# Kernel tuning notes

Measured on AMD Instinct MI355X. Metric: run time of the kernel, lower is better.

## Reference

```python
import jax, jax.numpy as jnp
import numpy as np

B, H, W, C = 64, 56, 56, 128
HEADS, WS, SHIFT = 4, 7, 3
HID = 4 * C
EPS = 1e-5
WS2 = WS * WS
DH = C // HEADS
# padding per torch code: [P_l, P_r, P_t, P_b] = [ws-shift, shift, ws-shift, shift]
P_L, P_R, P_T, P_B = WS - SHIFT, SHIFT, WS - SHIFT, SHIFT
_H, _W = H + P_T + P_B, W + P_L + P_R  # 63, 63


def layer_norm(x, g, b):
    mu = jnp.mean(x, axis=-1, keepdims=True)
    xc = x - mu
    var = jnp.mean(xc * xc, axis=-1, keepdims=True)
    return xc * jax.lax.rsqrt(var + EPS) * g + b


def setup_inputs() -> dict:
    key = jax.random.key(0)
    ks = jax.random.split(key, 12)
    s = 0.02
    return {
        "x": jax.random.normal(ks[0], (B, H * W, C), jnp.float32),
        "g1": jnp.ones((C,), jnp.float32),
        "b1": jnp.zeros((C,), jnp.float32),
        "spatial_w": jax.random.normal(ks[1], (HEADS, WS2, WS2), jnp.float32) * s,
        "spatial_b": jnp.zeros((HEADS, WS2), jnp.float32),
        "g2": jnp.ones((C,), jnp.float32),
        "b2": jnp.zeros((C,), jnp.float32),
        "fc1_w": jax.random.normal(ks[2], (C, HID), jnp.float32) * s,
        "fc1_b": jnp.zeros((HID,), jnp.float32),
        "fc2_w": jax.random.normal(ks[3], (HID, C), jnp.float32) * s,
        "fc2_b": jnp.zeros((C,), jnp.float32),
    }


def reference(x, g1, b1, spatial_w, spatial_b, g2, b2, fc1_w, fc1_b, fc2_w, fc2_b):
    shortcut = x
    xn = layer_norm(x, g1, b1).reshape(B, H, W, C)
    # shifted padding (shift_size > 0 branch)
    xp = jnp.pad(xn, ((0, 0), (P_T, P_B), (P_L, P_R), (0, 0)))  # (B,_H,_W,C)
    nh, nw = _H // WS, _W // WS
    # window_partition -> (B*nh*nw, WS*WS, C)
    xw = xp.reshape(B, nh, WS, nw, WS, C).transpose(0, 1, 3, 2, 4, 5).reshape(-1, WS2, C)
    # split heads: (nWB, HEADS, WS2, DH)
    xh = xw.reshape(-1, WS2, HEADS, DH).transpose(0, 2, 1, 3)
    # grouped 1x1 Conv1d == per-head token-mixing matmul over the WS2 axis
    yh = jnp.einsum("bhjd,hij->bhid", xh, spatial_w) + spatial_b[None, :, :, None]
    yw = yh.transpose(0, 2, 1, 3).reshape(-1, WS2, C)
    # window_reverse -> (B,_H,_W,C), then crop the shift padding
    y = yw.reshape(B, nh, nw, WS, WS, C).transpose(0, 1, 3, 2, 4, 5).reshape(B, _H, _W, C)
    y = y[:, P_T:_H - P_B, P_L:_W - P_R, :].reshape(B, H * W, C)
    x = shortcut + y
    # channel MLP with exact (erf) GELU as in F.gelu
    h = layer_norm(x, g2, b2)
    h = jax.nn.gelu(h @ fc1_w + fc1_b, approximate=False)
    x = x + (h @ fc2_w + fc2_b)
    return x
```

## Files before the change

### kernel.cpp

```cpp
#include <hip/hip_runtime.h>

typedef unsigned short u16;
typedef __attribute__((ext_vector_type(8))) short short8;
typedef __attribute__((ext_vector_type(4))) float floatx4;

#define NB 64
#define HH 56
#define WW_ 56
#define CC 128
#define NHEADS 4
#define WS2 49
#define PAD 4
#define HID 512

__device__ __forceinline__ float bf2f(u16 u){ return __uint_as_float(((unsigned)u)<<16); }
__device__ __forceinline__ u16 f2bf(float f){
  unsigned u = __float_as_uint(f);
  return (u16)((u + 0x7FFFu + ((u>>16)&1u)) >> 16);
}
__device__ __forceinline__ unsigned pk2(float a, float b){
  return ((unsigned)f2bf(b) << 16) | (unsigned)f2bf(a);
}
__device__ __forceinline__ float gelu_f(float x){
  float u2 = x*(1.5957691216f + 0.0713548162f*x*x);
  return x / (1.f + __expf(-u2));
}
__device__ __forceinline__ short8 ld_frag(const u16* p){
  short8 v;
  #pragma unroll
  for (int e = 0; e < 8; e++) v[e] = (short)p[e];
  return v;
}

__global__ __launch_bounds__(256) void prep_k(
    const float* __restrict__ fc1_w, const float* __restrict__ fc2_w,
    const float* __restrict__ sw,
    u16* __restrict__ fc1_wT, u16* __restrict__ fc2_wT, u16* __restrict__ swT)
{
  int tid = blockIdx.x*256 + threadIdx.x;
  int nth = gridDim.x * 256;
  for (int idx = tid; idx < HID*CC; idx += nth) {
    int n = idx >> 7, k = idx & 127;
    fc1_wT[idx] = f2bf(fc1_w[k*HID + n]);
  }
  for (int idx = tid; idx < CC*HID; idx += nth) {
    int c = idx >> 9, h = idx & 511;
    fc2_wT[idx] = f2bf(fc2_w[h*CC + c]);
  }
  for (int idx = tid; idx < NHEADS*64*72; idx += nth) {
    int hd = idx / (64*72); int rem = idx - hd*64*72;
    int i = rem / 72, j = rem - i*72;
    swT[idx] = (i < WS2 && j < WS2) ? f2bf(sw[(hd*WS2 + i)*WS2 + j]) : (u16)0;
  }
}

__global__ __launch_bounds__(256, 3) void winmix_k(
    const float* __restrict__ x, const float* __restrict__ g1, const float* __restrict__ b1,
    const u16* __restrict__ swT, const float* __restrict__ sb,
    float* __restrict__ x2)
{
  __shared__ __align__(16) char uw[NHEADS*64*72*2];
  __shared__ float sbl[NHEADS*WS2];
  u16* wl  = (u16*)uw;
  u16* xnt = (u16*)uw;
  int tid = threadIdx.x;
  int wvid = tid >> 6, lane = tid & 63;
  int ln = lane & 15, qd = lane >> 4;
  int b = blockIdx.x / 81; int wi = blockIdx.x - b*81;
  int wh = wi / 9, wwn = wi - wh*9;

  {
    const uint2* ws = (const uint2*)swT;
    uint2* wd = (uint2*)wl;
    #pragma unroll
    for (int r = 0; r < 18; r++) wd[tid + r*256] = ws[tid + r*256];
    if (tid < NHEADS*WS2) sbl[tid] = sb[tid];
  }
  __syncthreads();

  int hd = wvid;
  const u16* wbase = wl + hd*64*72;
  short8 af[4][2];
  #pragma unroll
  for (int mt = 0; mt < 4; mt++)
    #pragma unroll
    for (int ks = 0; ks < 2; ks++)
      af[mt][ks] = ld_frag(&wbase[(mt*16 + ln)*72 + ks*32 + qd*8]);
  __syncthreads();

  float gl0 = g1[lane], gl1 = g1[lane+64];
  float bl0 = b1[lane], bl1 = b1[lane+64];
  for (int jj = wvid; jj < 64; jj += 4) {
    u16 o0 = 0, o1 = 0;
    if (jj < WS2) {
      int jr = jj / 7, jc = jj - jr*7;
      int pr = wh*7 + jr - PAD, pc = wwn*7 + jc - PAD;
      bool valid = (pr>=0) & (pr<HH) & (pc>=0) & (pc<WW_);
      float v0 = 0.f, v1 = 0.f;
      const float* px = x + ((size_t)((b*HH + pr)*WW_ + pc))*CC;
      if (valid) { v0 = px[lane]; v1 = px[lane+64]; }
      float s = v0 + v1, ss = v0*v0 + v1*v1;
      #pragma unroll
      for (int o = 32; o > 0; o >>= 1) { s += __shfl_xor(s, o); ss += __shfl_xor(ss, o); }
      float mu = s * (1.f/128.f);
      float var = ss * (1.f/128.f) - mu*mu;
      float rs = rsqrtf(var + 1e-5f);
      if (valid) {
        o0 = f2bf((v0 - mu)*rs*gl0 + bl0);
        o1 = f2bf((v1 - mu)*rs*gl1 + bl1);
      }
    }
    xnt[lane*66 + jj]      = o0;
    xnt[(lane+64)*66 + jj] = o1;
  }
  __syncthreads();

  short8 bf_[2][2];
  #pragma unroll
  for (int nt = 0; nt < 2; nt++)
    #pragma unroll
    for (int ks = 0; ks < 2; ks++)
      bf_[nt][ks] = ld_frag(&xnt[(hd*32 + nt*16 + ln)*66 + ks*32 + qd*8]);
  floatx4 acc[4][2];
  #pragma unroll
  for (int mt = 0; mt < 4; mt++)
    #pragma unroll
    for (int nt = 0; nt < 2; nt++)
      acc[mt][nt] = (floatx4){0.f,0.f,0.f,0.f};
  #pragma unroll
  for (int ks = 0; ks < 2; ks++)
    #pragma unroll
    for (int mt = 0; mt < 4; mt++)
      #pragma unroll
      for (int nt = 0; nt < 2; nt++)
        acc[mt][nt] = __builtin_amdgcn_mfma_f32_16x16x32_bf16(af[mt][ks], bf_[nt][ks], acc[mt][nt], 0, 0, 0);

  #pragma unroll
  for (int mt = 0; mt < 4; mt++) {
    #pragma unroll
    for (int r = 0; r < 4; r++) {
      int i = mt*16 + qd*4 + r;
      if (i < WS2) {
        int ir = i / 7, ic = i - ir*7;
        int orow = wh*7 + ir - PAD, ocol = wwn*7 + ic - PAD;
        if (orow>=0 && orow<HH && ocol>=0 && ocol<WW_) {
          float sbv = sbl[hd*WS2 + i];
          size_t base = ((size_t)((b*HH + orow)*WW_ + ocol))*CC + hd*32;
          #pragma unroll
          for (int nt = 0; nt < 2; nt++) {
            int c = nt*16 + ln;
            x2[base + c] = x[base + c] + acc[mt][nt][r] + sbv;
          }
        }
      }
    }
  }
}

__global__ __launch_bounds__(256, 3) void mlp_k(
    float* __restrict__ xio,
    const float* __restrict__ g2, const float* __restrict__ b2,
    const u16* __restrict__ fc1_wT, const float* __restrict__ fc1_b,
    const u16* __restrict__ fc2_wT, const float* __restrict__ fc2_b)
{
  __shared__ __align__(16) char um[53248];
  u16* ALn = (u16*)um;
  u16* B1p = (u16*)um;
  u16* B2p = (u16*)(um + 17408);
  int tid = threadIdx.x;
  int wvid = tid >> 6, lane = tid & 63;
  int ln = lane & 15, qd = lane >> 4;
  int m0 = wvid*32;
  size_t tokbase = (size_t)blockIdx.x * 128;
  u16* Htp = (u16*)(um + 35840) + wvid*(32*68);

  const uint4* src1 = (const uint4*)fc1_wT;
  const uint4* src2 = (const uint4*)fc2_wT;
  uint4 p1[4], p2[4];
  int n1[4], q1[4], n2[4], q2[4];
  #pragma unroll
  for (int r = 0; r < 4; r++) {
    int idx = tid + r*256;
    n1[r] = idx >> 4; q1[r] = idx & 15;
    n2[r] = idx >> 3; q2[r] = idx & 7;
  }
  auto load_ch = [&](int cc){
    #pragma unroll
    for (int r = 0; r < 4; r++) {
      p1[r] = src1[(cc*64 + n1[r])*16 + q1[r]];
      p2[r] = src2[n2[r]*64 + cc*8 + q2[r]];
    }
  };
  auto store_ch = [&](){
    uint4* d1 = (uint4*)B1p; uint4* d2 = (uint4*)B2p;
    #pragma unroll
    for (int r = 0; r < 4; r++) {
      d1[n1[r]*17 + q1[r]] = p1[r];
      d2[n2[r]*9  + q2[r]] = p2[r];
    }
  };
  load_ch(0);

  float2 gl = *(const float2*)&g2[2*lane];
  float2 bl = *(const float2*)&b2[2*lane];
  for (int t = wvid; t < 128; t += 4) {
    float2 v = *(const float2*)(xio + (tokbase + t)*CC + 2*lane);
    float s = v.x + v.y, ss = v.x*v.x + v.y*v.y;
    #pragma unroll
    for (int o = 32; o > 0; o >>= 1) { s += __shfl_xor(s,o); ss += __shfl_xor(ss,o); }
    float mu = s*(1.f/128.f), var = ss*(1.f/128.f) - mu*mu;
    float rs = rsqrtf(var + 1e-5f);
    *(unsigned*)&ALn[t*136 + 2*lane] =
        pk2((v.x-mu)*rs*gl.x + bl.x, (v.y-mu)*rs*gl.y + bl.y);
  }
  __syncthreads();

  short8 bv[2][4];
  #pragma unroll
  for (int n = 0; n < 2; n++)
    #pragma unroll
    for (int ks = 0; ks < 4; ks++)
      bv[n][ks] = ld_frag(&ALn[(m0 + n*16 + ln)*136 + ks*32 + qd*8]);
  __syncthreads();

  store_ch();
  __syncthreads();

  floatx4 oacc[2][8];
  #pragma unroll
  for (int mt = 0; mt < 2; mt++)
    #pragma unroll
    for (int nt = 0; nt < 8; nt++) oacc[mt][nt] = (floatx4){0.f,0.f,0.f,0.f};

  for (int ch = 0; ch < 8; ch++) {
    if (ch < 7) load_ch(ch+1);

    #pragma unroll
    for (int kt = 0; kt < 4; ++kt) {
      short8 aw[4];
      #pragma unroll
      for (int ks = 0; ks < 4; ks++)
        aw[ks] = ld_frag(&B1p[(kt*16 + ln)*136 + ks*32 + qd*8]);
      floatx4 h0 = (floatx4){0.f,0.f,0.f,0.f};
      floatx4 h1 = (floatx4){0.f,0.f,0.f,0.f};
      #pragma unroll
      for (int ks = 0; ks < 4; ks++) {
        h0 = __builtin_amdgcn_mfma_f32_16x16x32_bf16(aw[ks], bv[0][ks], h0, 0, 0, 0);
        h1 = __builtin_amdgcn_mfma_f32_16x16x32_bf16(aw[ks], bv[1][ks], h1, 0, 0, 0);
      }
      floatx4 bias = *(const floatx4*)&fc1_b[ch*64 + kt*16 + qd*4];
      uint2 u0, u1;
      u0.x = pk2(gelu_f(h0[0]+bias[0]), gelu_f(h0[1]+bias[1]));
      u0.y = pk2(gelu_f(h0[2]+bias[2]), gelu_f(h0[3]+bias[3]));
      u1.x = pk2(gelu_f(h1[0]+bias[0]), gelu_f(h1[1]+bias[1]));
      u1.y = pk2(gelu_f(h1[2]+bias[2]), gelu_f(h1[3]+bias[3]));
      *(uint2*)&Htp[(     ln)*68 + kt*16 + qd*4] = u0;
      *(uint2*)&Htp[(16 + ln)*68 + kt*16 + qd*4] = u1;
    }

    short8 av2[2][2];
    #pragma unroll
    for (int mt = 0; mt < 2; mt++)
      #pragma unroll
      for (int ks = 0; ks < 2; ks++)
        av2[mt][ks] = ld_frag(&Htp[(mt*16 + ln)*68 + ks*32 + qd*8]);
    #pragma unroll
    for (int nt = 0; nt < 8; nt++) {
      short8 bv2[2];
      #pragma unroll
      for (int ks = 0; ks < 2; ks++)
        bv2[ks] = ld_frag(&B2p[(nt*16 + ln)*72 + ks*32 + qd*8]);
      #pragma unroll
      for (int mt = 0; mt < 2; mt++)
        #pragma unroll
        for (int ks = 0; ks < 2; ks++)
          oacc[mt][nt] = __builtin_amdgcn_mfma_f32_16x16x32_bf16(av2[mt][ks], bv2[ks], oacc[mt][nt], 0, 0, 0);
    }
    __syncthreads();
    if (ch < 7) { store_ch(); __syncthreads(); }
  }

  float bias2[8];
  #pragma unroll
  for (int nt = 0; nt < 8; nt++) bias2[nt] = fc2_b[nt*16 + ln];
  #pragma unroll
  for (int mt = 0; mt < 2; mt++)
    #pragma unroll
    for (int r = 0; r < 4; r++) {
      size_t tok = tokbase + m0 + mt*16 + qd*4 + r;
      float* rowp = xio + tok*CC;
      #pragma unroll
      for (int nt = 0; nt < 8; nt++) {
        int n = nt*16 + ln;
        rowp[n] = rowp[n] + oacc[mt][nt][r] + bias2[nt];
      }
    }
}

extern "C" void kernel_launch(void* const* d_in, const int* in_sizes, int n_in,
                              void* d_out, int out_size, void* d_ws, size_t ws_size,
                              hipStream_t stream) {
  const float* x     = (const float*)d_in[0];
  const float* g1    = (const float*)d_in[1];
  const float* b1    = (const float*)d_in[2];
  const float* sw    = (const float*)d_in[3];
  const float* sb    = (const float*)d_in[4];
  const float* g2    = (const float*)d_in[5];
  const float* b2    = (const float*)d_in[6];
  const float* fc1_w = (const float*)d_in[7];
  const float* fc1_b = (const float*)d_in[8];
  const float* fc2_w = (const float*)d_in[9];
  const float* fc2_b = (const float*)d_in[10];
  float* out = (float*)d_out;

  u16* fc1_wT = (u16*)d_ws;
  u16* fc2_wT = fc1_wT + HID*CC;
  u16* swT    = fc2_wT + CC*HID;

  prep_k<<<64, 256, 0, stream>>>(fc1_w, fc2_w, sw, fc1_wT, fc2_wT, swT);
  winmix_k<<<NB*81, 256, 0, stream>>>(x, g1, b1, swT, sb, out);
  mlp_k<<<(NB*HH*WW_)/128, 256, 0, stream>>>(out, g2, b2, fc1_wT, fc1_b, fc2_wT, fc2_b);
}
```

Baseline: 500.6 us.

## Keep GELU output in registers for fc2 MFMA and drop LDS staging

The MLP kernel now packs the GELU results into bf16 MFMA B-operands directly in registers, using the hardware pack-convert instruction. This removes the per-wave LDS hidden-tile write and read-back, and the fc2 accumulator is transposed so the output can be written with vector floatx4 stores. The winmix kernel loads its mixing weights straight from global memory instead of staging them in LDS and reads the bias from global, with the weight padding changed to 80. LDS is smaller, but occupancy hints shift (mlp 3 to 2, winmix 3 to 4), and the GELU division becomes a reciprocal multiply with slightly different rounding.

Result: slower. 531.7 us (+6.2%).

```diff
diff --git a/kernel.cpp b/kernel.cpp
--- a/kernel.cpp
+++ b/kernel.cpp
@@ -2,6 +2,8 @@
 
 typedef unsigned short u16;
 typedef __attribute__((ext_vector_type(8))) short short8;
+typedef __attribute__((ext_vector_type(4))) short short4v;
+typedef __attribute__((ext_vector_type(2))) unsigned uint2v;
 typedef __attribute__((ext_vector_type(4))) float floatx4;
 
 #define NB 64
@@ -21,14 +23,36 @@
 __device__ __forceinline__ unsigned pk2(float a, float b){
   return ((unsigned)f2bf(b) << 16) | (unsigned)f2bf(a);
 }
+__device__ __forceinline__ short4v pk4(float a, float b, float c, float d){
+  unsigned w0, w1;
+  asm("v_cvt_pk_bf16_f32 %0, %1, %2" : "=v"(w0) : "v"(a), "v"(b));
+  asm("v_cvt_pk_bf16_f32 %0, %1, %2" : "=v"(w1) : "v"(c), "v"(d));
+  uint2v u; u[0] = w0; u[1] = w1;
+  return __builtin_bit_cast(short4v, u);
+}
 __device__ __forceinline__ float gelu_f(float x){
   float u2 = x*(1.5957691216f + 0.0713548162f*x*x);
-  return x / (1.f + __expf(-u2));
+  return x * __builtin_amdgcn_rcpf(1.f + __expf(-u2));
 }
 __device__ __forceinline__ short8 ld_frag(const u16* p){
   short8 v;
   #pragma unroll
   for (int e = 0; e < 8; e++) v[e] = (short)p[e];
+  return v;
+}
+__device__ __forceinline__ short4v ld_frag4(const u16* p){
+  short4v v;
+  #pragma unroll
+  for (int e = 0; e < 4; e++) v[e] = (short)p[e];
+  return v;
+}
+__device__ __forceinline__ short8 ld_frag_g(const u16* p){
+  return *(const short8*)p;
+}
+__device__ __forceinline__ short8 cat8(short4v lo, short4v hi){
+  short8 v;
+  #pragma unroll
+  for (int e = 0; e < 4; e++) { v[e] = lo[e]; v[e+4] = hi[e]; }
   return v;
 }
 
@@ -47,71 +71,57 @@
     int c = idx >> 9, h = idx & 511;
     fc2_wT[idx] = f2bf(fc2_w[h*CC + c]);
   }
-  for (int idx = tid; idx < NHEADS*64*72; idx += nth) {
-    int hd = idx / (64*72); int rem = idx - hd*64*72;
-    int i = rem / 72, j = rem - i*72;
+  for (int idx = tid; idx < NHEADS*64*80; idx += nth) {
+    int hd = idx / (64*80); int rem = idx - hd*64*80;
+    int i = rem / 80, j = rem - i*80;
     swT[idx] = (i < WS2 && j < WS2) ? f2bf(sw[(hd*WS2 + i)*WS2 + j]) : (u16)0;
   }
 }
 
-__global__ __launch_bounds__(256, 3) void winmix_k(
+__global__ __launch_bounds__(256, 4) void winmix_k(
     const float* __restrict__ x, const float* __restrict__ g1, const float* __restrict__ b1,
     const u16* __restrict__ swT, const float* __restrict__ sb,
     float* __restrict__ x2)
 {
-  __shared__ __align__(16) char uw[NHEADS*64*72*2];
-  __shared__ float sbl[NHEADS*WS2];
-  u16* wl  = (u16*)uw;
-  u16* xnt = (u16*)uw;
+  __shared__ u16 xnt[CC*66];
   int tid = threadIdx.x;
   int wvid = tid >> 6, lane = tid & 63;
   int ln = lane & 15, qd = lane >> 4;
   int b = blockIdx.x / 81; int wi = blockIdx.x - b*81;
   int wh = wi / 9, wwn = wi - wh*9;
-
-  {
-    const uint2* ws = (const uint2*)swT;
-    uint2* wd = (uint2*)wl;
-    #pragma unroll
-    for (int r = 0; r < 18; r++) wd[tid + r*256] = ws[tid + r*256];
-    if (tid < NHEADS*WS2) sbl[tid] = sb[tid];
-  }
-  __syncthreads();
-
   int hd = wvid;
-  const u16* wbase = wl + hd*64*72;
+
   short8 af[4][2];
   #pragma unroll
   for (int mt = 0; mt < 4; mt++)
     #pragma unroll
     for (int ks = 0; ks < 2; ks++)
-      af[mt][ks] = ld_frag(&wbase[(mt*16 + ln)*72 + ks*32 + qd*8]);
-  __syncthreads();
-
-  float gl0 = g1[lane], gl1 = g1[lane+64];
-  float bl0 = b1[lane], bl1 = b1[lane+64];
+      af[mt][ks] = ld_frag_g(&swT[(size_t)(hd*64 + mt*16 + ln)*80 + ks*32 + qd*8]);
+
+  float2 gl = *(const float2*)&g1[2*lane];
+  float2 bl = *(const float2*)&b1[2*lane];
   for (int jj = wvid; jj < 64; jj += 4) {
     u16 o0 = 0, o1 = 0;
     if (jj < WS2) {
       int jr = jj / 7, jc = jj - jr*7;
       int pr = wh*7 + jr - PAD, pc = wwn*7 + jc - PAD;
       bool valid = (pr>=0) & (pr<HH) & (pc>=0) & (pc<WW_);
-      float v0 = 0.f, v1 = 0.f;
+      float2 v = {0.f, 0.f};
       const float* px = x + ((size_t)((b*HH + pr)*WW_ + pc))*CC;
-      if (valid) { v0 = px[lane]; v1 = px[lane+64]; }
-      float s = v0 + v1, ss = v0*v0 + v1*v1;
+      if (valid) v = *(const float2*)(px + 2*lane);
+      float s = v.x + v.y, ss = v.x*v.x + v.y*v.y;
       #pragma unroll
       for (int o = 32; o > 0; o >>= 1) { s += __shfl_xor(s, o); ss += __shfl_xor(ss, o); }
       float mu = s * (1.f/128.f);
       float var = ss * (1.f/128.f) - mu*mu;
       float rs = rsqrtf(var + 1e-5f);
       if (valid) {
-        o0 = f2bf((v0 - mu)*rs*gl0 + bl0);
-        o1 = f2bf((v1 - mu)*rs*gl1 + bl1);
+        o0 = f2bf((v.x - mu)*rs*gl.x + bl.x);
+        o1 = f2bf((v.y - mu)*rs*gl.y + bl.y);
       }
     }
-    xnt[lane*66 + jj]      = o0;
-    xnt[(lane+64)*66 + jj] = o1;
+    xnt[(2*lane  )*66 + jj] = o0;
+    xnt[(2*lane+1)*66 + jj] = o1;
   }
   __syncthreads();
 
@@ -144,7 +154,7 @@
         int ir = i / 7, ic = i - ir*7;
         int orow = wh*7 + ir - PAD, ocol = wwn*7 + ic - PAD;
         if (orow>=0 && orow<HH && ocol>=0 && ocol<WW_) {
-          float sbv = sbl[hd*WS2 + i];
+          float sbv = sb[hd*WS2 + i];
           size_t base = ((size_t)((b*HH + orow)*WW_ + ocol))*CC + hd*32;
           #pragma unroll
           for (int nt = 0; nt < 2; nt++) {
@@ -157,13 +167,13 @@
   }
 }
 
-__global__ __launch_bounds__(256, 3) void mlp_k(
+__global__ __launch_bounds__(256, 2) void mlp_k(
     float* __restrict__ xio,
     const float* __restrict__ g2, const float* __restrict__ b2,
     const u16* __restrict__ fc1_wT, const float* __restrict__ fc1_b,
     const u16* __restrict__ fc2_wT, const float* __restrict__ fc2_b)
 {
-  __shared__ __align__(16) char um[53248];
+  __shared__ __align__(16) char um[35840];
   u16* ALn = (u16*)um;
   u16* B1p = (u16*)um;
   u16* B2p = (u16*)(um + 17408);
@@ -172,7 +182,6 @@
   int ln = lane & 15, qd = lane >> 4;
   int m0 = wvid*32;
   size_t tokbase = (size_t)blockIdx.x * 128;
-  u16* Htp = (u16*)(um + 35840) + wvid*(32*68);
 
   const uint4* src1 = (const uint4*)fc1_wT;
   const uint4* src2 = (const uint4*)fc2_wT;
@@ -226,75 +235,64 @@
   store_ch();
   __syncthreads();
 
-  floatx4 oacc[2][8];
-  #pragma unroll
-  for (int mt = 0; mt < 2; mt++)
-    #pragma unroll
-    for (int nt = 0; nt < 8; nt++) oacc[mt][nt] = (floatx4){0.f,0.f,0.f,0.f};
+  floatx4 oacc[8][2];
+  #pragma unroll
+  for (int nt = 0; nt < 8; nt++)
+    #pragma unroll
+    for (int th = 0; th < 2; th++) oacc[nt][th] = (floatx4){0.f,0.f,0.f,0.f};
 
   for (int ch = 0; ch < 8; ch++) {
     if (ch < 7) load_ch(ch+1);
 
     #pragma unroll
-    for (int kt = 0; kt < 4; ++kt) {
-      short8 aw[4];
+    for (int kb = 0; kb < 2; ++kb) {
+      short4v pkv[2][2];
       #pragma unroll
-      for (int ks = 0; ks < 4; ks++)
-        aw[ks] = ld_frag(&B1p[(kt*16 + ln)*136 + ks*32 + qd*8]);
-      floatx4 h0 = (floatx4){0.f,0.f,0.f,0.f};
-      floatx4 h1 = (floatx4){0.f,0.f,0.f,0.f};
+      for (int kp = 0; kp < 2; ++kp) {
+        int kt = kb*2 + kp;
+        short8 aw[4];
+        #pragma unroll
+        for (int ks = 0; ks < 4; ks++)
+          aw[ks] = ld_frag(&B1p[(kt*16 + ln)*136 + ks*32 + qd*8]);
+        floatx4 h0 = (floatx4){0.f,0.f,0.f,0.f};
+        floatx4 h1 = (floatx4){0.f,0.f,0.f,0.f};
+        #pragma unroll
+        for (int ks = 0; ks < 4; ks++) {
+          h0 = __builtin_amdgcn_mfma_f32_16x16x32_bf16(aw[ks], bv[0][ks], h0, 0, 0, 0);
+          h1 = __builtin_amdgcn_mfma_f32_16x16x32_bf16(aw[ks], bv[1][ks], h1, 0, 0, 0);
+        }
+        floatx4 bias = *(const floatx4*)&fc1_b[ch*64 + kt*16 + qd*4];
+        pkv[kp][0] = pk4(gelu_f(h0[0]+bias[0]), gelu_f(h0[1]+bias[1]),
+                         gelu_f(h0[2]+bias[2]), gelu_f(h0[3]+bias[3]));
+        pkv[kp][1] = pk4(gelu_f(h1[0]+bias[0]), gelu_f(h1[1]+bias[1]),
+                         gelu_f(h1[2]+bias[2]), gelu_f(h1[3]+bias[3]));
+      }
+      short8 g0 = cat8(pkv[0][0], pkv[1][0]);
+      short8 g1 = cat8(pkv[0][1], pkv[1][1]);
       #pragma unroll
-      for (int ks = 0; ks < 4; ks++) {
-        h0 = __builtin_amdgcn_mfma_f32_16x16x32_bf16(aw[ks], bv[0][ks], h0, 0, 0, 0);
-        h1 = __builtin_amdgcn_mfma_f32_16x16x32_bf16(aw[ks], bv[1][ks], h1, 0, 0, 0);
+      for (int nt = 0; nt < 8; nt++) {
+        const u16* wrow = &B2p[(nt*16 + ln)*72 + kb*32 + qd*4];
+        short8 aw2 = cat8(ld_frag4(wrow), ld_frag4(wrow + 16));
+        oacc[nt][0] = __builtin_amdgcn_mfma_f32_16x16x32_bf16(aw2, g0, oacc[nt][0], 0, 0, 0);
+        oacc[nt][1] = __builtin_amdgcn_mfma_f32_16x16x32_bf16(aw2, g1, oacc[nt][1], 0, 0, 0);
       }
-      floatx4 bias = *(const floatx4*)&fc1_b[ch*64 + kt*16 + qd*4];
-      uint2 u0, u1;
-      u0.x = pk2(gelu_f(h0[0]+bias[0]), gelu_f(h0[1]+bias[1]));
-      u0.y = pk2(gelu_f(h0[2]+bias[2]), gelu_f(h0[3]+bias[3]));
-      u1.x = pk2(gelu_f(h1[0]+bias[0]), gelu_f(h1[1]+bias[1]));
-      u1.y = pk2(gelu_f(h1[2]+bias[2]), gelu_f(h1[3]+bias[3]));
-      *(uint2*)&Htp[(     ln)*68 + kt*16 + qd*4] = u0;
-      *(uint2*)&Htp[(16 + ln)*68 + kt*16 + qd*4] = u1;
-    }
-
-    short8 av2[2][2];
-    #pragma unroll
-    for (int mt = 0; mt < 2; mt++)
-      #pragma unroll
-      for (int ks = 0; ks < 2; ks++)
-        av2[mt][ks] = ld_frag(&Htp[(mt*16 + ln)*68 + ks*32 + qd*8]);
-    #pragma unroll
-    for (int nt = 0; nt < 8; nt++) {
-      short8 bv2[2];
-      #pragma unroll
-      for (int ks = 0; ks < 2; ks++)
-        bv2[ks] = ld_frag(&B2p[(nt*16 + ln)*72 + ks*32 + qd*8]);
-      #pragma unroll
-      for (int mt = 0; mt < 2; mt++)
-        #pragma unroll
-        for (int ks = 0; ks < 2; ks++)
-          oacc[mt][nt] = __builtin_amdgcn_mfma_f32_16x16x32_bf16(av2[mt][ks], bv2[ks], oacc[mt][nt], 0, 0, 0);
     }
     __syncthreads();
     if (ch < 7) { store_ch(); __syncthreads(); }
   }
 
-  float bias2[8];
-  #pragma unroll
-  for (int nt = 0; nt < 8; nt++) bias2[nt] = fc2_b[nt*16 + ln];
-  #pragma unroll
-  for (int mt = 0; mt < 2; mt++)
-    #pragma unroll
-    for (int r = 0; r < 4; r++) {
-      size_t tok = tokbase + m0 + mt*16 + qd*4 + r;
-      float* rowp = xio + tok*CC;
-      #pragma unroll
-      for (int nt = 0; nt < 8; nt++) {
-        int n = nt*16 + ln;
-        rowp[n] = rowp[n] + oacc[mt][nt][r] + bias2[nt];
-      }
-    }
+  #pragma unroll
+  for (int nt = 0; nt < 8; nt++) {
+    floatx4 bias = *(const floatx4*)&fc2_b[nt*16 + qd*4];
+    #pragma unroll
+    for (int th = 0; th < 2; th++) {
+      size_t tok = tokbase + m0 + th*16 + ln;
+      float* rp = xio + tok*CC + nt*16 + qd*4;
+      floatx4 v = *(floatx4*)rp;
+      v = v + oacc[nt][th] + bias;
+      *(floatx4*)rp = v;
+    }
+  }
 }
 
 extern "C" void kernel_launch(void* const* d_in, const int* in_sizes, int n_in,
```
